# Kernel tuning notes

Measured on AMD Instinct MI355X. Metric: run time of the kernel, lower is better.

Reference implementation:

```python
import jax, jax.numpy as jnp
import numpy as np

D_MODEL = 1024
D_STATE = 16
DT_RANK = 64  # d_model // 16 ('auto')
DT_MIN = 0.001
DT_MAX = 0.1


def setup_inputs() -> dict:
    key = jax.random.key(0)
    ks = jax.random.split(key, 7)
    B, S = 2, 2048
    return {
        "x": jax.random.normal(ks[0], (B, S, D_MODEL), jnp.float32),
        "w_in": jax.random.normal(ks[1], (D_MODEL, D_MODEL), jnp.float32) / np.sqrt(D_MODEL).astype(np.float32),
        "w_x": jax.random.normal(ks[2], (D_MODEL, DT_RANK + 2 * D_STATE), jnp.float32) / np.sqrt(D_MODEL).astype(np.float32),
        "w_dt": jax.random.normal(ks[3], (DT_RANK, D_MODEL), jnp.float32) / np.sqrt(DT_RANK).astype(np.float32),
        "b_dt": jnp.zeros((D_MODEL,), jnp.float32),
        "A_log": jax.random.normal(ks[5], (D_MODEL, D_STATE), jnp.float32) * 0.5,
        "Dp": jax.random.normal(ks[6], (D_MODEL,), jnp.float32),
    }


def reference(x, w_in, w_x, w_dt, b_dt, A_log, Dp):
    # x: (b, s, d)
    x_in = jnp.einsum('bsd,de->bse', x, w_in)          # in_proj, (b,s,d_inner=d)
    proj = jnp.einsum('bsd,dp->bsp', x_in, w_x)        # x_proj, (b,s,dt_rank+2n)
    dt_low, Bm, Cm = jnp.split(proj, [DT_RANK, DT_RANK + D_STATE], axis=-1)
    # dt_proj + softplus + range scaling -> (b,s,d)
    dt = jax.nn.softplus(jnp.einsum('bsr,rd->bsd', dt_low, w_dt) + b_dt) * (DT_MAX - DT_MIN) + DT_MIN
    A = -jnp.exp(A_log)                                # (d, n), strictly negative

    b, s, d = x.shape
    h0 = jnp.zeros((b, d, D_STATE), x.dtype)

    # time-major streams for scan
    dt_tm = jnp.swapaxes(dt, 0, 1)     # (s,b,d)
    u_tm = jnp.swapaxes(x_in, 0, 1)    # (s,b,d)
    B_tm = jnp.swapaxes(Bm, 0, 1)      # (s,b,n)
    C_tm = jnp.swapaxes(Cm, 0, 1)      # (s,b,n)

    def step(h, inp):
        dtt, ut, bt, ct = inp
        dA = dtt[:, :, None] * A                      # (b,d,n) = dt[b,d]*A[d,n]
        barA = jnp.exp(dA)
        # bar_B = dA; source sums the input term over channel dim d (keepdim)
        inp_term = jnp.einsum('bdn,bn,bd->bn', dA, bt, ut)  # (b,n)
        h = barA * h + inp_term[:, None, :]           # broadcast over d
        y = jnp.einsum('bdn,bn->bd', h, ct) + Dp * ut # (b,d)
        return h, y

    _, ys = jax.lax.scan(step, h0, (dt_tm, u_tm, B_tm, C_tm))  # ys: (s,b,d)
    return jnp.swapaxes(ys, 0, 1)                     # (b,s,d)
```

## Files before the change

### kernel.cpp

```cpp
#include <hip/hip_runtime.h>
#include <hip/hip_bf16.h>

#define D_MODEL 1024
#define D_STATE 16
#define DT_RANK 64
#define SEQ 2048
#define BATCH 2
#define M_TOTAL 4096
#define CHUNKS 64
#define CLEN 32
#define LOG2E 1.44269504088896f

typedef __bf16 bf16x8 __attribute__((ext_vector_type(8)));
typedef float f32x4 __attribute__((ext_vector_type(4)));

__device__ __forceinline__ unsigned short f2bf(float f) {
    union { float f; unsigned int u; } v; v.f = f;
    unsigned int r = v.u + 0x7FFFu + ((v.u >> 16) & 1u);
    return (unsigned short)(r >> 16);
}
__device__ __forceinline__ float bf2f(unsigned short u) {
    union { unsigned int i; float f; } v; v.i = ((unsigned int)u) << 16; return v.f;
}
__device__ __forceinline__ void gload16(const void* g, void* l) {
    __builtin_amdgcn_global_load_lds(
        (const __attribute__((address_space(1))) unsigned int*)g,
        (__attribute__((address_space(3))) unsigned int*)l, 16, 0, 0);
}
__device__ __forceinline__ float fexp2(float x) { return __builtin_amdgcn_exp2f(x); }

__global__ void __launch_bounds__(256) k_setup(const float* __restrict__ x,
                                               const float* __restrict__ win,
                                               const float* __restrict__ wx,
                                               const float* __restrict__ wdt,
                                               const float* __restrict__ alog,
                                               unsigned short* __restrict__ xb,
                                               unsigned short* __restrict__ bt,
                                               unsigned short* __restrict__ wxT,
                                               unsigned short* __restrict__ wxBC,
                                               unsigned short* __restrict__ wdtT,
                                               float* __restrict__ aneg,
                                               unsigned short* __restrict__ anegT) {
    __shared__ float tile[32][33];
    int blk = blockIdx.x;
    int t = threadIdx.x;
    if (blk < 4096) {
        int i = blk * 256 + t;
        float4 v = reinterpret_cast<const float4*>(x)[i];
        ushort4 o;
        o.x = f2bf(v.x); o.y = f2bf(v.y); o.z = f2bf(v.z); o.w = f2bf(v.w);
        reinterpret_cast<ushort4*>(xb)[i] = o;
    } else if (blk < 5120) {
        int blk2 = blk - 4096;
        int bx = blk2 & 31, by = blk2 >> 5;
        int tx = t & 31, ty = t >> 5;
        int xc = bx * 32 + tx;
#pragma unroll
        for (int j = 0; j < 4; j++)
            tile[ty + 8 * j][tx] = win[(by * 32 + ty + 8 * j) * D_MODEL + xc];
        __syncthreads();
        int x2 = by * 32 + tx;
#pragma unroll
        for (int j = 0; j < 4; j++)
            bt[(bx * 32 + ty + 8 * j) * D_MODEL + x2] = f2bf(tile[tx][ty + 8 * j]);
    } else if (blk < 5376) {
        int idx = (blk - 5120) * 256 + t;
        int e = idx & 1023, p = idx >> 10;
        wxT[p * D_MODEL + e] = f2bf(wx[e * 96 + p]);
    } else if (blk < 5504) {
        int idx = (blk - 5376) * 256 + t;
        int e = idx & 1023, p = idx >> 10;
        wxBC[p * D_MODEL + e] = f2bf(wx[e * 96 + 64 + p]);
    } else if (blk < 5568) {
        int i = (blk - 5504) * 256 + t;
        float v = -expf(alog[i]);
        aneg[i] = v * LOG2E;
        anegT[(i & 15) * D_MODEL + (i >> 4)] = f2bf(v);
    } else {
        int idx = (blk - 5568) * 256 + t;
        int d = idx & 1023, k = idx >> 10;
        wdtT[d * DT_RANK + k] = f2bf(wdt[k * D_MODEL + d]);
    }
}

__global__ void __launch_bounds__(256) k_gemm_xin(const unsigned short* __restrict__ xb,
                                                  const unsigned short* __restrict__ bt,
                                                  unsigned short* __restrict__ xinb) {
    __shared__ unsigned short sA[2][64 * 64];
    __shared__ unsigned short sB[2][128 * 64];
    int bid0 = blockIdx.x;
    int bid = (bid0 & 7) * 64 + (bid0 >> 3);
    int m0 = (bid >> 3) * 64;
    int n0 = (bid & 7) * 128;
    int t = threadIdx.x;
    int lane = t & 63;
    int w = t >> 6;
    int wm = (w >> 1) * 32, wn = (w & 1) * 64;
    int c = lane & 15, q = lane >> 4;

    const unsigned short* gA[2];
    const unsigned short* gB[4];
#pragma unroll
    for (int L = 0; L < 2; L++) {
        int s = L * 256 + t;
        int row = s >> 3, ch = (s & 7) ^ (row & 7);
        gA[L] = xb + (m0 + row) * D_MODEL + ch * 8;
    }
#pragma unroll
    for (int L = 0; L < 4; L++) {
        int s = L * 256 + t;
        int row = s >> 3, ch = (s & 7) ^ (row & 7);
        gB[L] = bt + (n0 + row) * D_MODEL + ch * 8;
    }

    f32x4 acc[2][4] = {};
    {
        char* la = (char*)&sA[0][0] + w * 1024;
        char* lb = (char*)&sB[0][0] + w * 1024;
#pragma unroll
        for (int L = 0; L < 2; L++) gload16(gA[L], la + L * 4096);
#pragma unroll
        for (int L = 0; L < 4; L++) gload16(gB[L], lb + L * 4096);
    }
    int cur = 0;
    for (int it = 0; it < 16; it++) {
        __syncthreads();
        if (it + 1 < 16) {
            int kn = (it + 1) * 64;
            char* la = (char*)&sA[cur ^ 1][0] + w * 1024;
            char* lb = (char*)&sB[cur ^ 1][0] + w * 1024;
#pragma unroll
            for (int L = 0; L < 2; L++) gload16(gA[L] + kn, la + L * 4096);
#pragma unroll
            for (int L = 0; L < 4; L++) gload16(gB[L] + kn, lb + L * 4096);
        }
#pragma unroll
        for (int kk = 0; kk < 2; kk++) {
            int perm = (((kk << 2) | q) ^ (c & 7)) << 3;
            bf16x8 af[2], bfr[4];
#pragma unroll
            for (int i = 0; i < 2; i++)
                af[i] = *reinterpret_cast<const bf16x8*>(&sA[cur][(wm + i * 16 + c) * 64 + perm]);
#pragma unroll
            for (int j = 0; j < 4; j++)
                bfr[j] = *reinterpret_cast<const bf16x8*>(&sB[cur][(wn + j * 16 + c) * 64 + perm]);
#pragma unroll
            for (int i = 0; i < 2; i++)
#pragma unroll
                for (int j = 0; j < 4; j++)
                    acc[i][j] = __builtin_amdgcn_mfma_f32_16x16x32_bf16(bfr[j], af[i], acc[i][j], 0, 0, 0);
        }
        cur ^= 1;
    }
#pragma unroll
    for (int i = 0; i < 2; i++) {
        int row = m0 + wm + i * 16 + c;
#pragma unroll
        for (int j = 0; j < 4; j++) {
            int col = n0 + wn + j * 16 + q * 4;
            ushort4 o;
            o.x = f2bf(acc[i][j][0]); o.y = f2bf(acc[i][j][1]);
            o.z = f2bf(acc[i][j][2]); o.w = f2bf(acc[i][j][3]);
            *reinterpret_cast<ushort4*>(&xinb[row * D_MODEL + col]) = o;
        }
    }
}

__global__ void __launch_bounds__(256) k_dt2(const unsigned short* __restrict__ xinb,
                                             const unsigned short* __restrict__ wxT,
                                             const unsigned short* __restrict__ wdtT,
                                             const float* __restrict__ bdt,
                                             unsigned short* __restrict__ dtb) {
    __shared__ float sP[4][64][17];
    __shared__ unsigned short sX[16 * 64];
    int m0 = blockIdx.x * 16;
    int t = threadIdx.x;
    int lane = t & 63, w = t >> 6;
    int c = lane & 15, q = lane >> 4;

    f32x4 acc[4] = {};
    const unsigned short* pa = xinb + (m0 + c) * D_MODEL + w * 256 + q * 8;
    const unsigned short* pw = wxT + c * D_MODEL + w * 256 + q * 8;
#pragma unroll
    for (int k0 = 0; k0 < 256; k0 += 32) {
        bf16x8 a0 = *reinterpret_cast<const bf16x8*>(pa + k0);
#pragma unroll
        for (int j = 0; j < 4; j++) {
            bf16x8 wf = *reinterpret_cast<const bf16x8*>(pw + j * 16 * D_MODEL + k0);
            acc[j] = __builtin_amdgcn_mfma_f32_16x16x32_bf16(wf, a0, acc[j], 0, 0, 0);
        }
    }
#pragma unroll
    for (int j = 0; j < 4; j++)
#pragma unroll
        for (int r = 0; r < 4; r++)
            sP[w][j * 16 + q * 4 + r][c] = acc[j][r];
    __syncthreads();

    {
        int m = t >> 4, col4 = t & 15;
        float s0 = 0.f, s1 = 0.f, s2 = 0.f, s3 = 0.f;
#pragma unroll
        for (int ww = 0; ww < 4; ww++) {
            s0 += sP[ww][col4 * 4 + 0][m];
            s1 += sP[ww][col4 * 4 + 1][m];
            s2 += sP[ww][col4 * 4 + 2][m];
            s3 += sP[ww][col4 * 4 + 3][m];
        }
        ushort4 o;
        o.x = f2bf(s0); o.y = f2bf(s1); o.z = f2bf(s2); o.w = f2bf(s3);
        int chunk = col4 >> 1, within = (col4 & 1) * 4;
        int swz = chunk ^ (m & 7);
        *reinterpret_cast<ushort4*>(&sX[m * 64 + swz * 8 + within]) = o;
    }
    __syncthreads();

    bf16x8 af[2];
#pragma unroll
    for (int kk = 0; kk < 2; kk++) {
        int swz = (kk * 4 + q) ^ (c & 7);
        af[kk] = *reinterpret_cast<const bf16x8*>(&sX[c * 64 + swz * 8]);
    }
    int nbase = w * 256;
#pragma unroll 4
    for (int j = 0; j < 16; j++) {
        f32x4 a = {};
#pragma unroll
        for (int kk = 0; kk < 2; kk++) {
            bf16x8 bfr = *reinterpret_cast<const bf16x8*>(
                &wdtT[(nbase + j * 16 + c) * DT_RANK + kk * 32 + q * 8]);
            a = __builtin_amdgcn_mfma_f32_16x16x32_bf16(bfr, af[kk], a, 0, 0, 0);
        }
        int dcol = nbase + j * 16 + q * 4;
        float4 bv = *reinterpret_cast<const float4*>(&bdt[dcol]);
        ushort4 o;
        {
            float xv = a[0] + bv.x;
            float sp = fmaxf(xv, 0.f) + __logf(1.f + __expf(-fabsf(xv)));
            o.x = f2bf(sp * 0.099f + 0.001f);
        }
        {
            float xv = a[1] + bv.y;
            float sp = fmaxf(xv, 0.f) + __logf(1.f + __expf(-fabsf(xv)));
            o.y = f2bf(sp * 0.099f + 0.001f);
        }
        {
            float xv = a[2] + bv.z;
            float sp = fmaxf(xv, 0.f) + __logf(1.f + __expf(-fabsf(xv)));
            o.z = f2bf(sp * 0.099f + 0.001f);
        }
        {
            float xv = a[3] + bv.w;
            float sp = fmaxf(xv, 0.f) + __logf(1.f + __expf(-fabsf(xv)));
            o.w = f2bf(sp * 0.099f + 0.001f);
        }
        *reinterpret_cast<ushort4*>(&dtb[(m0 + c) * D_MODEL + dcol]) = o;
    }
}

__global__ void __launch_bounds__(256) k_bcw(const unsigned short* __restrict__ xinb,
                                             const unsigned short* __restrict__ dtb,
                                             const unsigned short* __restrict__ wxBC,
                                             const unsigned short* __restrict__ anegT,
                                             float* __restrict__ bcp,
                                             float* __restrict__ wpp) {
    int bid = blockIdx.x;
    int m0 = (bid & 31) * 128;
    int ks = bid >> 5;
    int kbase = ks * 128;
    int t = threadIdx.x;
    int lane = t & 63, w = t >> 6;
    int c = lane & 15, q = lane >> 4;
    int mw = m0 + w * 32;
    f32x4 accb[2][2] = {};
    f32x4 accw[2] = {};
    const unsigned short* pa0 = xinb + (mw + c) * D_MODEL + kbase + q * 8;
    const unsigned short* pa1 = pa0 + 16 * D_MODEL;
    const unsigned short* pt0 = dtb + (mw + c) * D_MODEL + kbase + q * 8;
    const unsigned short* pt1 = pt0 + 16 * D_MODEL;
    const unsigned short* pb0 = wxBC + c * D_MODEL + kbase + q * 8;
    const unsigned short* pb1 = pb0 + 16 * D_MODEL;
    const unsigned short* pA = anegT + c * D_MODEL + kbase + q * 8;
#pragma unroll
    for (int k0 = 0; k0 < 128; k0 += 32) {
        bf16x8 a0 = *reinterpret_cast<const bf16x8*>(pa0 + k0);
        bf16x8 a1 = *reinterpret_cast<const bf16x8*>(pa1 + k0);
        bf16x8 t0 = *reinterpret_cast<const bf16x8*>(pt0 + k0);
        bf16x8 t1 = *reinterpret_cast<const bf16x8*>(pt1 + k0);
        bf16x8 b0 = *reinterpret_cast<const bf16x8*>(pb0 + k0);
        bf16x8 b1 = *reinterpret_cast<const bf16x8*>(pb1 + k0);
        bf16x8 bA = *reinterpret_cast<const bf16x8*>(pA + k0);
        bf16x8 g0, g1;
#pragma unroll
        for (int e = 0; e < 8; e++) {
            g0[e] = (__bf16)((float)t0[e] * (float)a0[e]);
            g1[e] = (__bf16)((float)t1[e] * (float)a1[e]);
        }
        accb[0][0] = __builtin_amdgcn_mfma_f32_16x16x32_bf16(b0, a0, accb[0][0], 0, 0, 0);
        accb[0][1] = __builtin_amdgcn_mfma_f32_16x16x32_bf16(b1, a0, accb[0][1], 0, 0, 0);
        accb[1][0] = __builtin_amdgcn_mfma_f32_16x16x32_bf16(b0, a1, accb[1][0], 0, 0, 0);
        accb[1][1] = __builtin_amdgcn_mfma_f32_16x16x32_bf16(b1, a1, accb[1][1], 0, 0, 0);
        accw[0] = __builtin_amdgcn_mfma_f32_16x16x32_bf16(bA, g0, accw[0], 0, 0, 0);
        accw[1] = __builtin_amdgcn_mfma_f32_16x16x32_bf16(bA, g1, accw[1], 0, 0, 0);
    }
#pragma unroll
    for (int i = 0; i < 2; i++) {
        int row = mw + i * 16 + c;
#pragma unroll
        for (int j = 0; j < 2; j++)
            *reinterpret_cast<f32x4*>(&bcp[(ks * M_TOTAL + row) * 32 + j * 16 + q * 4]) = accb[i][j];
        *reinterpret_cast<f32x4*>(&wpp[(ks * M_TOTAL + row) * 16 + q * 4]) = accw[i];
    }
}

__global__ void __launch_bounds__(256) k_scan1(const unsigned short* __restrict__ dtb,
                                               const float* __restrict__ bcp,
                                               const float* __restrict__ wpp,
                                               const float* __restrict__ aneg,
                                               float* __restrict__ h_loc,
                                               float* __restrict__ dtsum) {
    __shared__ unsigned short s_dt[16][256];
    __shared__ float s_w[16][16];
    int bid0 = blockIdx.x;
    int bid = (bid0 & 7) * 64 + (bid0 >> 3);
    int dc = bid & 3;
    int c = (bid >> 2) & (CHUNKS - 1);
    int b = bid >> 8;
    int tid = threadIdx.x;
    int d = dc * 256 + tid;
    float Ad[16];
    const float4* ar = reinterpret_cast<const float4*>(aneg + d * 16);
#pragma unroll
    for (int j = 0; j < 4; j++) {
        float4 a4 = ar[j];
        Ad[4 * j + 0] = a4.x; Ad[4 * j + 1] = a4.y;
        Ad[4 * j + 2] = a4.z; Ad[4 * j + 3] = a4.w;
    }
    float h[16];
#pragma unroll
    for (int n = 0; n < 16; n++) h[n] = 0.f;
    float dts = 0.f;

    int r8 = tid >> 5, col8 = (tid & 31) * 8;
    for (int t0 = 0; t0 < CLEN; t0 += 16) {
        __syncthreads();
        int rowbase = b * SEQ + c * CLEN + t0;
        *reinterpret_cast<uint4*>(&s_dt[r8][col8]) =
            *reinterpret_cast<const uint4*>(dtb + (rowbase + r8) * D_MODEL + dc * 256 + col8);
        *reinterpret_cast<uint4*>(&s_dt[8 + r8][col8]) =
            *reinterpret_cast<const uint4*>(dtb + (rowbase + 8 + r8) * D_MODEL + dc * 256 + col8);
        {
            int r = tid >> 4, n = tid & 15;
            int row = rowbase + r;
            float sB = 0.f, sw = 0.f;
#pragma unroll
            for (int ks = 0; ks < 8; ks++) {
                sB += bcp[(ks * M_TOTAL + row) * 32 + n];
                sw += wpp[(ks * M_TOTAL + row) * 16 + n];
            }
            s_w[r][n] = sB * sw;
        }
        __syncthreads();
        for (int r = 0; r < 16; r++) {
            float dtv = bf2f(s_dt[r][tid]);
            dts += dtv;
#pragma unroll
            for (int n = 0; n < 16; n++) {
                float ba = fexp2(dtv * Ad[n]);
                h[n] = fmaf(ba, h[n], s_w[r][n]);
            }
        }
    }
    int base = ((b * CHUNKS + c) * D_MODEL + d) * 16;
#pragma unroll
    for (int j = 0; j < 4; j++) {
        f32x4 v = {h[4 * j], h[4 * j + 1], h[4 * j + 2], h[4 * j + 3]};
        *reinterpret_cast<f32x4*>(h_loc + base + 4 * j) = v;
    }
    dtsum[(b * CHUNKS + c) * D_MODEL + d] = dts;
}

__global__ void __launch_bounds__(128) k_scan2(float* __restrict__ h_inout,
                                               const float* __restrict__ dtsum,
                                               const float* __restrict__ aneg) {
    int idx = blockIdx.x * 128 + threadIdx.x;
    int n = idx & 15;
    int d = (idx >> 4) & (D_MODEL - 1);
    int b = idx >> 14;
    float A = aneg[d * 16 + n];
    float H = 0.f;
    int off0 = b * CHUNKS * D_MODEL + d;
#pragma unroll 1
    for (int g = 0; g < CHUNKS; g += 8) {
        float hl[8], ds[8];
#pragma unroll
        for (int j = 0; j < 8; j++) {
            int off = off0 + (g + j) * D_MODEL;
            hl[j] = h_inout[off * 16 + n];
            ds[j] = dtsum[off];
        }
#pragma unroll
        for (int j = 0; j < 8; j++) {
            int off = off0 + (g + j) * D_MODEL;
            float P = fexp2(ds[j] * A);
            h_inout[off * 16 + n] = H;
            H = fmaf(P, H, hl[j]);
        }
    }
}

__global__ void __launch_bounds__(256) k_scan3(const unsigned short* __restrict__ dtb,
                                               const unsigned short* __restrict__ xinb,
                                               const float* __restrict__ bcp,
                                               const float* __restrict__ wpp,
                                               const float* __restrict__ aneg,
                                               const float* __restrict__ dp,
                                               const float* __restrict__ H_in,
                                               float* __restrict__ out) {
    __shared__ unsigned short s_dt[16][256], s_u[16][256];
    __shared__ float s_w[16][16], s_c[16][16];
    int bid0 = blockIdx.x;
    int bid = (bid0 & 7) * 64 + (bid0 >> 3);
    int dc = bid & 3;
    int c = (bid >> 2) & (CHUNKS - 1);
    int b = bid >> 8;
    int tid = threadIdx.x;
    int d = dc * 256 + tid;
    float Ad[16];
    const float4* ar = reinterpret_cast<const float4*>(aneg + d * 16);
#pragma unroll
    for (int j = 0; j < 4; j++) {
        float4 a4 = ar[j];
        Ad[4 * j + 0] = a4.x; Ad[4 * j + 1] = a4.y;
        Ad[4 * j + 2] = a4.z; Ad[4 * j + 3] = a4.w;
    }
    float Dpd = dp[d];
    float h[16];
    int base = ((b * CHUNKS + c) * D_MODEL + d) * 16;
#pragma unroll
    for (int j = 0; j < 4; j++) {
        f32x4 v = *reinterpret_cast<const f32x4*>(H_in + base + 4 * j);
        h[4 * j] = v[0]; h[4 * j + 1] = v[1]; h[4 * j + 2] = v[2]; h[4 * j + 3] = v[3];
    }

    int r8 = tid >> 5, col8 = (tid & 31) * 8;
    for (int t0 = 0; t0 < CLEN; t0 += 16) {
        __syncthreads();
        int rowbase = b * SEQ + c * CLEN + t0;
        *reinterpret_cast<uint4*>(&s_dt[r8][col8]) =
            *reinterpret_cast<const uint4*>(dtb + (rowbase + r8) * D_MODEL + dc * 256 + col8);
        *reinterpret_cast<uint4*>(&s_dt[8 + r8][col8]) =
            *reinterpret_cast<const uint4*>(dtb + (rowbase + 8 + r8) * D_MODEL + dc * 256 + col8);
        *reinterpret_cast<uint4*>(&s_u[r8][col8]) =
            *reinterpret_cast<const uint4*>(xinb + (rowbase + r8) * D_MODEL + dc * 256 + col8);
        *reinterpret_cast<uint4*>(&s_u[8 + r8][col8]) =
            *reinterpret_cast<const uint4*>(xinb + (rowbase + 8 + r8) * D_MODEL + dc * 256 + col8);
        {
            int r = tid >> 4, n = tid & 15;
            int row = rowbase + r;
            float sB = 0.f, sw = 0.f, sC = 0.f;
#pragma unroll
            for (int ks = 0; ks < 8; ks++) {
                sB += bcp[(ks * M_TOTAL + row) * 32 + n];
                sC += bcp[(ks * M_TOTAL + row) * 32 + 16 + n];
                sw += wpp[(ks * M_TOTAL + row) * 16 + n];
            }
            s_w[r][n] = sB * sw;
            s_c[r][n] = sC;
        }
        __syncthreads();
        for (int r = 0; r < 16; r++) {
            float dtv = bf2f(s_dt[r][tid]), uv = bf2f(s_u[r][tid]);
            float y = Dpd * uv;
#pragma unroll
            for (int n = 0; n < 16; n++) {
                float ba = fexp2(dtv * Ad[n]);
                h[n] = fmaf(ba, h[n], s_w[r][n]);
                y = fmaf(h[n], s_c[r][n], y);
            }
            out[(rowbase + r) * D_MODEL + d] = y;
        }
    }
}

extern "C" void kernel_launch(void* const* d_in, const int* in_sizes, int n_in,
                              void* d_out, int out_size, void* d_ws, size_t ws_size,
                              hipStream_t stream) {
    const float* x     = (const float*)d_in[0];
    const float* w_in  = (const float*)d_in[1];
    const float* w_x   = (const float*)d_in[2];
    const float* w_dt  = (const float*)d_in[3];
    const float* b_dt  = (const float*)d_in[4];
    const float* A_log = (const float*)d_in[5];
    const float* Dp    = (const float*)d_in[6];
    float* out = (float*)d_out;

    char* ws = (char*)d_ws;
    unsigned short* xb   = (unsigned short*)(ws + 0);
    unsigned short* bt   = (unsigned short*)(ws + 8388608);
    unsigned short* xinb = (unsigned short*)(ws + 10485760);
    unsigned short* dtb  = (unsigned short*)(ws + 18874368);
    float* bcp           = (float*)(ws + 27262976);
    float* wpp           = (float*)(ws + 31457280);
    unsigned short* wxT  = (unsigned short*)(ws + 35651584);
    unsigned short* wxBC = (unsigned short*)(ws + 35782656);
    unsigned short* wdtT = (unsigned short*)(ws + 35848192);
    float* aneg          = (float*)(ws + 35979264);
    unsigned short* anegT= (unsigned short*)(ws + 36044800);
    float* h_loc         = (float*)(ws + 0);
    float* dtsum         = (float*)(ws + 8388608);

    k_setup<<<5824, 256, 0, stream>>>(x, w_in, w_x, w_dt, A_log, xb, bt, wxT, wxBC, wdtT, aneg, anegT);
    k_gemm_xin<<<512, 256, 0, stream>>>(xb, bt, xinb);
    k_dt2<<<256, 256, 0, stream>>>(xinb, wxT, wdtT, b_dt, dtb);
    k_bcw<<<256, 256, 0, stream>>>(xinb, dtb, wxBC, anegT, bcp, wpp);
    k_scan1<<<BATCH * CHUNKS * 4, 256, 0, stream>>>(dtb, bcp, wpp, aneg, h_loc, dtsum);
    k_scan2<<<256, 128, 0, stream>>>(h_loc, dtsum, aneg);
    k_scan3<<<BATCH * CHUNKS * 4, 256, 0, stream>>>(dtb, xinb, bcp, wpp, aneg, Dp, h_loc, out);
}
```

Before: 159.9 us.

## Fuse dt projection with B/C/w projection and drop split-K partial buffers

Merges the dt kernel and the B/C/input-weight kernel into one kernel. Each block projects B, C and the dt-weighted term for its own 16 rows over the full reduction dimension, combining the per-wave partials in shared memory. It then writes the final product B·w and C directly instead of eight split-K partial buffers. The two scan kernels now read one value per element instead of re-reducing the eight partials. This removes a launch and several MB of partial-buffer traffic. The cost is that the fused kernel re-reads from global the dt values it just wrote, and the B/C work is spread over fewer blocks than before.

```diff
diff --git a/kernel.cpp b/kernel.cpp
--- a/kernel.cpp
+++ b/kernel.cpp
@@ -166,35 +166,42 @@
     }
 }
 
-__global__ void __launch_bounds__(256) k_dt2(const unsigned short* __restrict__ xinb,
-                                             const unsigned short* __restrict__ wxT,
-                                             const unsigned short* __restrict__ wdtT,
-                                             const float* __restrict__ bdt,
-                                             unsigned short* __restrict__ dtb) {
+__global__ void __launch_bounds__(256) k_dtbcw(const unsigned short* __restrict__ xinb,
+                                               const unsigned short* __restrict__ wxT,
+                                               const unsigned short* __restrict__ wdtT,
+                                               const float* __restrict__ bdt,
+                                               const unsigned short* __restrict__ wxBC,
+                                               const unsigned short* __restrict__ anegT,
+                                               unsigned short* __restrict__ dtb,
+                                               float* __restrict__ winp,
+                                               float* __restrict__ bcC) {
     __shared__ float sP[4][64][17];
     __shared__ unsigned short sX[16 * 64];
+    __shared__ float sBC[4][16][49];
     int m0 = blockIdx.x * 16;
     int t = threadIdx.x;
     int lane = t & 63, w = t >> 6;
     int c = lane & 15, q = lane >> 4;
 
-    f32x4 acc[4] = {};
-    const unsigned short* pa = xinb + (m0 + c) * D_MODEL + w * 256 + q * 8;
-    const unsigned short* pw = wxT + c * D_MODEL + w * 256 + q * 8;
-#pragma unroll
-    for (int k0 = 0; k0 < 256; k0 += 32) {
-        bf16x8 a0 = *reinterpret_cast<const bf16x8*>(pa + k0);
-#pragma unroll
-        for (int j = 0; j < 4; j++) {
-            bf16x8 wf = *reinterpret_cast<const bf16x8*>(pw + j * 16 * D_MODEL + k0);
-            acc[j] = __builtin_amdgcn_mfma_f32_16x16x32_bf16(wf, a0, acc[j], 0, 0, 0);
-        }
-    }
-#pragma unroll
-    for (int j = 0; j < 4; j++)
-#pragma unroll
-        for (int r = 0; r < 4; r++)
-            sP[w][j * 16 + q * 4 + r][c] = acc[j][r];
+    {
+        f32x4 acc[4] = {};
+        const unsigned short* pa = xinb + (m0 + c) * D_MODEL + w * 256 + q * 8;
+        const unsigned short* pw = wxT + c * D_MODEL + w * 256 + q * 8;
+#pragma unroll
+        for (int k0 = 0; k0 < 256; k0 += 32) {
+            bf16x8 a0 = *reinterpret_cast<const bf16x8*>(pa + k0);
+#pragma unroll
+            for (int j = 0; j < 4; j++) {
+                bf16x8 wf = *reinterpret_cast<const bf16x8*>(pw + j * 16 * D_MODEL + k0);
+                acc[j] = __builtin_amdgcn_mfma_f32_16x16x32_bf16(wf, a0, acc[j], 0, 0, 0);
+            }
+        }
+#pragma unroll
+        for (int j = 0; j < 4; j++)
+#pragma unroll
+            for (int r = 0; r < 4; r++)
+                sP[w][j * 16 + q * 4 + r][c] = acc[j][r];
+    }
     __syncthreads();
 
     {
@@ -215,107 +222,100 @@
     }
     __syncthreads();
 
-    bf16x8 af[2];
-#pragma unroll
-    for (int kk = 0; kk < 2; kk++) {
-        int swz = (kk * 4 + q) ^ (c & 7);
-        af[kk] = *reinterpret_cast<const bf16x8*>(&sX[c * 64 + swz * 8]);
-    }
-    int nbase = w * 256;
+    {
+        bf16x8 af[2];
+#pragma unroll
+        for (int kk = 0; kk < 2; kk++) {
+            int swz = (kk * 4 + q) ^ (c & 7);
+            af[kk] = *reinterpret_cast<const bf16x8*>(&sX[c * 64 + swz * 8]);
+        }
+        int nbase = w * 256;
 #pragma unroll 4
-    for (int j = 0; j < 16; j++) {
-        f32x4 a = {};
-#pragma unroll
-        for (int kk = 0; kk < 2; kk++) {
-            bf16x8 bfr = *reinterpret_cast<const bf16x8*>(
-                &wdtT[(nbase + j * 16 + c) * DT_RANK + kk * 32 + q * 8]);
-            a = __builtin_amdgcn_mfma_f32_16x16x32_bf16(bfr, af[kk], a, 0, 0, 0);
-        }
-        int dcol = nbase + j * 16 + q * 4;
-        float4 bv = *reinterpret_cast<const float4*>(&bdt[dcol]);
-        ushort4 o;
-        {
-            float xv = a[0] + bv.x;
-            float sp = fmaxf(xv, 0.f) + __logf(1.f + __expf(-fabsf(xv)));
-            o.x = f2bf(sp * 0.099f + 0.001f);
-        }
-        {
-            float xv = a[1] + bv.y;
-            float sp = fmaxf(xv, 0.f) + __logf(1.f + __expf(-fabsf(xv)));
-            o.y = f2bf(sp * 0.099f + 0.001f);
-        }
-        {
-            float xv = a[2] + bv.z;
-            float sp = fmaxf(xv, 0.f) + __logf(1.f + __expf(-fabsf(xv)));
-            o.z = f2bf(sp * 0.099f + 0.001f);
-        }
-        {
-            float xv = a[3] + bv.w;
-            float sp = fmaxf(xv, 0.f) + __logf(1.f + __expf(-fabsf(xv)));
-            o.w = f2bf(sp * 0.099f + 0.001f);
-        }
-        *reinterpret_cast<ushort4*>(&dtb[(m0 + c) * D_MODEL + dcol]) = o;
-    }
-}
-
-__global__ void __launch_bounds__(256) k_bcw(const unsigned short* __restrict__ xinb,
-                                             const unsigned short* __restrict__ dtb,
-                                             const unsigned short* __restrict__ wxBC,
-                                             const unsigned short* __restrict__ anegT,
-                                             float* __restrict__ bcp,
-                                             float* __restrict__ wpp) {
-    int bid = blockIdx.x;
-    int m0 = (bid & 31) * 128;
-    int ks = bid >> 5;
-    int kbase = ks * 128;
-    int t = threadIdx.x;
-    int lane = t & 63, w = t >> 6;
-    int c = lane & 15, q = lane >> 4;
-    int mw = m0 + w * 32;
-    f32x4 accb[2][2] = {};
-    f32x4 accw[2] = {};
-    const unsigned short* pa0 = xinb + (mw + c) * D_MODEL + kbase + q * 8;
-    const unsigned short* pa1 = pa0 + 16 * D_MODEL;
-    const unsigned short* pt0 = dtb + (mw + c) * D_MODEL + kbase + q * 8;
-    const unsigned short* pt1 = pt0 + 16 * D_MODEL;
-    const unsigned short* pb0 = wxBC + c * D_MODEL + kbase + q * 8;
-    const unsigned short* pb1 = pb0 + 16 * D_MODEL;
-    const unsigned short* pA = anegT + c * D_MODEL + kbase + q * 8;
-#pragma unroll
-    for (int k0 = 0; k0 < 128; k0 += 32) {
-        bf16x8 a0 = *reinterpret_cast<const bf16x8*>(pa0 + k0);
-        bf16x8 a1 = *reinterpret_cast<const bf16x8*>(pa1 + k0);
-        bf16x8 t0 = *reinterpret_cast<const bf16x8*>(pt0 + k0);
-        bf16x8 t1 = *reinterpret_cast<const bf16x8*>(pt1 + k0);
-        bf16x8 b0 = *reinterpret_cast<const bf16x8*>(pb0 + k0);
-        bf16x8 b1 = *reinterpret_cast<const bf16x8*>(pb1 + k0);
-        bf16x8 bA = *reinterpret_cast<const bf16x8*>(pA + k0);
-        bf16x8 g0, g1;
-#pragma unroll
-        for (int e = 0; e < 8; e++) {
-            g0[e] = (__bf16)((float)t0[e] * (float)a0[e]);
-            g1[e] = (__bf16)((float)t1[e] * (float)a1[e]);
-        }
-        accb[0][0] = __builtin_amdgcn_mfma_f32_16x16x32_bf16(b0, a0, accb[0][0], 0, 0, 0);
-        accb[0][1] = __builtin_amdgcn_mfma_f32_16x16x32_bf16(b1, a0, accb[0][1], 0, 0, 0);
-        accb[1][0] = __builtin_amdgcn_mfma_f32_16x16x32_bf16(b0, a1, accb[1][0], 0, 0, 0);
-        accb[1][1] = __builtin_amdgcn_mfma_f32_16x16x32_bf16(b1, a1, accb[1][1], 0, 0, 0);
-        accw[0] = __builtin_amdgcn_mfma_f32_16x16x32_bf16(bA, g0, accw[0], 0, 0, 0);
-        accw[1] = __builtin_amdgcn_mfma_f32_16x16x32_bf16(bA, g1, accw[1], 0, 0, 0);
-    }
-#pragma unroll
-    for (int i = 0; i < 2; i++) {
-        int row = mw + i * 16 + c;
+        for (int j = 0; j < 16; j++) {
+            f32x4 a = {};
+#pragma unroll
+            for (int kk = 0; kk < 2; kk++) {
+                bf16x8 bfr = *reinterpret_cast<const bf16x8*>(
+                    &wdtT[(nbase + j * 16 + c) * DT_RANK + kk * 32 + q * 8]);
+                a = __builtin_amdgcn_mfma_f32_16x16x32_bf16(bfr, af[kk], a, 0, 0, 0);
+            }
+            int dcol = nbase + j * 16 + q * 4;
+            float4 bv = *reinterpret_cast<const float4*>(&bdt[dcol]);
+            ushort4 o;
+            {
+                float xv = a[0] + bv.x;
+                float sp = fmaxf(xv, 0.f) + __logf(1.f + __expf(-fabsf(xv)));
+                o.x = f2bf(sp * 0.099f + 0.001f);
+            }
+            {
+                float xv = a[1] + bv.y;
+                float sp = fmaxf(xv, 0.f) + __logf(1.f + __expf(-fabsf(xv)));
+                o.y = f2bf(sp * 0.099f + 0.001f);
+            }
+            {
+                float xv = a[2] + bv.z;
+                float sp = fmaxf(xv, 0.f) + __logf(1.f + __expf(-fabsf(xv)));
+                o.z = f2bf(sp * 0.099f + 0.001f);
+            }
+            {
+                float xv = a[3] + bv.w;
+                float sp = fmaxf(xv, 0.f) + __logf(1.f + __expf(-fabsf(xv)));
+                o.w = f2bf(sp * 0.099f + 0.001f);
+            }
+            *reinterpret_cast<ushort4*>(&dtb[(m0 + c) * D_MODEL + dcol]) = o;
+        }
+    }
+    __syncthreads();
+
+    {
+        f32x4 accb[2] = {};
+        f32x4 accw = {};
+        const unsigned short* pa = xinb + (m0 + c) * D_MODEL + w * 256 + q * 8;
+        const unsigned short* pt = dtb + (m0 + c) * D_MODEL + w * 256 + q * 8;
+        const unsigned short* pb0 = wxBC + c * D_MODEL + w * 256 + q * 8;
+        const unsigned short* pb1 = pb0 + 16 * D_MODEL;
+        const unsigned short* pA = anegT + c * D_MODEL + w * 256 + q * 8;
+#pragma unroll
+        for (int k0 = 0; k0 < 256; k0 += 32) {
+            bf16x8 a0 = *reinterpret_cast<const bf16x8*>(pa + k0);
+            bf16x8 t0 = *reinterpret_cast<const bf16x8*>(pt + k0);
+            bf16x8 b0 = *reinterpret_cast<const bf16x8*>(pb0 + k0);
+            bf16x8 b1 = *reinterpret_cast<const bf16x8*>(pb1 + k0);
+            bf16x8 bA = *reinterpret_cast<const bf16x8*>(pA + k0);
+            bf16x8 g0;
+#pragma unroll
+            for (int e = 0; e < 8; e++) g0[e] = (__bf16)((float)t0[e] * (float)a0[e]);
+            accb[0] = __builtin_amdgcn_mfma_f32_16x16x32_bf16(b0, a0, accb[0], 0, 0, 0);
+            accb[1] = __builtin_amdgcn_mfma_f32_16x16x32_bf16(b1, a0, accb[1], 0, 0, 0);
+            accw = __builtin_amdgcn_mfma_f32_16x16x32_bf16(bA, g0, accw, 0, 0, 0);
+        }
 #pragma unroll
         for (int j = 0; j < 2; j++)
-            *reinterpret_cast<f32x4*>(&bcp[(ks * M_TOTAL + row) * 32 + j * 16 + q * 4]) = accb[i][j];
-        *reinterpret_cast<f32x4*>(&wpp[(ks * M_TOTAL + row) * 16 + q * 4]) = accw[i];
+#pragma unroll
+            for (int r = 0; r < 4; r++)
+                sBC[w][c][j * 16 + q * 4 + r] = accb[j][r];
+#pragma unroll
+        for (int r = 0; r < 4; r++)
+            sBC[w][c][32 + q * 4 + r] = accw[r];
+    }
+    __syncthreads();
+
+    {
+        int row = t >> 4, n = t & 15;
+        float sB = 0.f, sC = 0.f, sW = 0.f;
+#pragma unroll
+        for (int ww = 0; ww < 4; ww++) {
+            sB += sBC[ww][row][n];
+            sC += sBC[ww][row][16 + n];
+            sW += sBC[ww][row][32 + n];
+        }
+        winp[(m0 + row) * 16 + n] = sB * sW;
+        bcC[(m0 + row) * 16 + n] = sC;
     }
 }
 
 __global__ void __launch_bounds__(256) k_scan1(const unsigned short* __restrict__ dtb,
-                                               const float* __restrict__ bcp,
-                                               const float* __restrict__ wpp,
+                                               const float* __restrict__ winp,
                                                const float* __restrict__ aneg,
                                                float* __restrict__ h_loc,
                                                float* __restrict__ dtsum) {
@@ -351,14 +351,7 @@
             *reinterpret_cast<const uint4*>(dtb + (rowbase + 8 + r8) * D_MODEL + dc * 256 + col8);
         {
             int r = tid >> 4, n = tid & 15;
-            int row = rowbase + r;
-            float sB = 0.f, sw = 0.f;
-#pragma unroll
-            for (int ks = 0; ks < 8; ks++) {
-                sB += bcp[(ks * M_TOTAL + row) * 32 + n];
-                sw += wpp[(ks * M_TOTAL + row) * 16 + n];
-            }
-            s_w[r][n] = sB * sw;
+            s_w[r][n] = winp[(rowbase + r) * 16 + n];
         }
         __syncthreads();
         for (int r = 0; r < 16; r++) {
@@ -411,8 +404,8 @@
 
 __global__ void __launch_bounds__(256) k_scan3(const unsigned short* __restrict__ dtb,
                                                const unsigned short* __restrict__ xinb,
-                                               const float* __restrict__ bcp,
-                                               const float* __restrict__ wpp,
+                                               const float* __restrict__ winp,
+                                               const float* __restrict__ bcC,
                                                const float* __restrict__ aneg,
                                                const float* __restrict__ dp,
                                                const float* __restrict__ H_in,
@@ -457,16 +450,8 @@
             *reinterpret_cast<const uint4*>(xinb + (rowbase + 8 + r8) * D_MODEL + dc * 256 + col8);
         {
             int r = tid >> 4, n = tid & 15;
-            int row = rowbase + r;
-            float sB = 0.f, sw = 0.f, sC = 0.f;
-#pragma unroll
-            for (int ks = 0; ks < 8; ks++) {
-                sB += bcp[(ks * M_TOTAL + row) * 32 + n];
-                sC += bcp[(ks * M_TOTAL + row) * 32 + 16 + n];
-                sw += wpp[(ks * M_TOTAL + row) * 16 + n];
-            }
-            s_w[r][n] = sB * sw;
-            s_c[r][n] = sC;
+            s_w[r][n] = winp[(rowbase + r) * 16 + n];
+            s_c[r][n] = bcC[(rowbase + r) * 16 + n];
         }
         __syncthreads();
         for (int r = 0; r < 16; r++) {
@@ -500,8 +485,8 @@
     unsigned short* bt   = (unsigned short*)(ws + 8388608);
     unsigned short* xinb = (unsigned short*)(ws + 10485760);
     unsigned short* dtb  = (unsigned short*)(ws + 18874368);
-    float* bcp           = (float*)(ws + 27262976);
-    float* wpp           = (float*)(ws + 31457280);
+    float* winp          = (float*)(ws + 27262976);
+    float* bcC           = (float*)(ws + 27525120);
     unsigned short* wxT  = (unsigned short*)(ws + 35651584);
     unsigned short* wxBC = (unsigned short*)(ws + 35782656);
     unsigned short* wdtT = (unsigned short*)(ws + 35848192);
@@ -512,9 +497,8 @@
 
     k_setup<<<5824, 256, 0, stream>>>(x, w_in, w_x, w_dt, A_log, xb, bt, wxT, wxBC, wdtT, aneg, anegT);
     k_gemm_xin<<<512, 256, 0, stream>>>(xb, bt, xinb);
-    k_dt2<<<256, 256, 0, stream>>>(xinb, wxT, wdtT, b_dt, dtb);
-    k_bcw<<<256, 256, 0, stream>>>(xinb, dtb, wxBC, anegT, bcp, wpp);
-    k_scan1<<<BATCH * CHUNKS * 4, 256, 0, stream>>>(dtb, bcp, wpp, aneg, h_loc, dtsum);
+    k_dtbcw<<<256, 256, 0, stream>>>(xinb, wxT, wdtT, b_dt, wxBC, anegT, dtb, winp, bcC);
+    k_scan1<<<BATCH * CHUNKS * 4, 256, 0, stream>>>(dtb, winp, aneg, h_loc, dtsum);
     k_scan2<<<256, 128, 0, stream>>>(h_loc, dtsum, aneg);
-    k_scan3<<<BATCH * CHUNKS * 4, 256, 0, stream>>>(dtb, xinb, bcp, wpp, aneg, Dp, h_loc, out);
-}
+    k_scan3<<<BATCH * CHUNKS * 4, 256, 0, stream>>>(dtb, xinb, winp, bcC, aneg, Dp, h_loc, out);
+}
```

Measured after the change: 153.3 us (median of 2 runs). -4.1%, faster.
